# Optimization experiments

Measured on AMD Instinct MI355X. Metric: run time of the kernel, lower is better.

The kernel has to match this reference:

```python
import jax, jax.numpy as jnp
import numpy as np

B, S, HID = 2, 2048, 2048
NH, HD, G = 16, 128, 4
NKV = NH // G  # 4
ROPE_THETA = 10000.0


def _xavier(key, shape):
    fan_in, fan_out = shape
    lim = float(np.sqrt(6.0 / (fan_in + fan_out)))
    return jax.random.uniform(key, shape, jnp.float32, -lim, lim)


def setup_inputs() -> dict:
    key = jax.random.key(0)
    ks = jax.random.split(key, 6)
    hidden_states = jax.random.normal(ks[0], (B, S, HID), jnp.float32)
    # mask==True means MASKED (code adds mask * -1e9): causal upper triangle
    causal = jnp.triu(jnp.ones((S, S), jnp.bool_), k=1)
    mask = jnp.broadcast_to(causal[None, None], (B, 1, S, S))
    return {
        "hidden_states": hidden_states,
        "mask": mask,
        "Wq": _xavier(ks[1], (HID, NH * HD)),
        "bq": jnp.zeros((NH * HD,), jnp.float32),
        "Wk": _xavier(ks[2], (HID, NKV * HD)),
        "bk": jnp.zeros((NKV * HD,), jnp.float32),
        "Wv": _xavier(ks[3], (HID, NKV * HD)),
        "bv": jnp.zeros((NKV * HD,), jnp.float32),
        "Wo": _xavier(ks[4], (NH * HD, HID)),
        "bo": jnp.zeros((HID,), jnp.float32),
    }


def _rope_cos_sin(seq_len, head_dim, dtype):
    half = head_dim // 2
    inv_freq = 1.0 / (ROPE_THETA ** (jnp.arange(0, half, dtype=jnp.float32) / half))
    ang = jnp.arange(seq_len, dtype=jnp.float32)[:, None] * inv_freq[None, :]  # [S, half]
    # shape [1, S, 1, half] for broadcasting over (B, S, H, half)
    return jnp.cos(ang)[None, :, None, :].astype(dtype), jnp.sin(ang)[None, :, None, :].astype(dtype)


def _apply_rope(x, cos, sin):
    half = x.shape[-1] // 2
    x1, x2 = x[..., :half], x[..., half:]
    return jnp.concatenate([x1 * cos - x2 * sin, x1 * sin + x2 * cos], axis=-1)


def reference(hidden_states, mask, Wq, bq, Wk, bk, Wv, bv, Wo, bo):
    b, s, _ = hidden_states.shape
    scale = 1.0 / jnp.sqrt(jnp.asarray(HD, hidden_states.dtype))

    q = (hidden_states @ Wq + bq).reshape(b, s, NH, HD)
    k = (hidden_states @ Wk + bk).reshape(b, s, NKV, HD)
    v = (hidden_states @ Wv + bv).reshape(b, s, NKV, HD)

    cos, sin = _rope_cos_sin(s, HD, hidden_states.dtype)
    q = _apply_rope(q, cos, sin)
    k = _apply_rope(k, cos, sin)

    q = jnp.transpose(q, (0, 2, 1, 3))          # [B, NH, S, D]
    k = jnp.transpose(k, (0, 2, 1, 3))          # [B, NKV, S, D]
    v = jnp.transpose(v, (0, 2, 1, 3))          # [B, NKV, S, D]

    # GQA: group query heads instead of repeating K/V (same math as jnp.repeat)
    qg = q.reshape(b, NKV, G, s, HD)
    scores = jnp.einsum('bngqd,bnkd->bngqk', qg, k) * scale  # [B, NKV, G, S, S]

    maskf = mask.astype(scores.dtype)[:, :, None]  # [B, 1, 1, S, S]
    scores = scores + maskf * (-1e9)

    probs = jax.nn.softmax(scores, axis=-1)
    out = jnp.einsum('bngqk,bnkd->bngqd', probs, v)          # [B, NKV, G, S, D]
    out = out.reshape(b, NH, s, HD).transpose(0, 2, 1, 3).reshape(b, s, NH * HD)
    return out @ Wo + bo
```

## Files before the change

kernel.cpp:

```cpp
#include <hip/hip_runtime.h>
#include <hip/hip_bf16.h>

#define B_ 2
#define S_ 2048
#define HID_ 2048
#define NH_ 16
#define HD_ 128
#define NKV_ 4
#define M_ (B_*S_)
#define NQKV_ 3072
#define QSCALE2 0.12752464484148957f
#define DEFER_THR 11.5425f
#define NSPLIT 4

typedef __bf16 bf16x8 __attribute__((ext_vector_type(8)));
typedef float f32x4 __attribute__((ext_vector_type(4)));
typedef float f32x16 __attribute__((ext_vector_type(16)));

typedef __attribute__((address_space(1))) const unsigned int gas_uint;
typedef __attribute__((address_space(3))) unsigned int las_uint;

__device__ __forceinline__ unsigned short f2bfu(float x) {
  __hip_bfloat16 h = __float2bfloat16(x);
  return __builtin_bit_cast(unsigned short, h);
}

__device__ __forceinline__ unsigned int pack2bf(float lo, float hi) {
  return (unsigned int)f2bfu(lo) | ((unsigned int)f2bfu(hi) << 16);
}

__device__ __forceinline__ float bflo(unsigned int u) {
  return __builtin_bit_cast(float, u << 16);
}
__device__ __forceinline__ float bfhi(unsigned int u) {
  return __builtin_bit_cast(float, u & 0xffff0000u);
}
__device__ __forceinline__ float bf2f(unsigned short u) {
  return __builtin_bit_cast(float, (unsigned int)u << 16);
}

__device__ __forceinline__ void gload_lds16(const void* g, void* l) {
  __builtin_amdgcn_global_load_lds((gas_uint*)g, (las_uint*)l, 16, 0, 0);
}


__global__ void k_prep(const float* __restrict__ X, unsigned short* __restrict__ Xb,
                       const float* __restrict__ bq, const float* __restrict__ bk,
                       const float* __restrict__ bv, float* __restrict__ Bqkv,
                       float* __restrict__ cosT, float* __restrict__ sinT) {
  int blk = blockIdx.x;
  if (blk < 8192) {
    int i = blk * 256 + threadIdx.x;
    float4 v = ((const float4*)X)[i];
    ushort4 o;
    o.x = f2bfu(v.x); o.y = f2bfu(v.y); o.z = f2bfu(v.z); o.w = f2bfu(v.w);
    ((ushort4*)Xb)[i] = o;
  } else if (blk < 8204) {
    int i = (blk - 8192) * 256 + threadIdx.x;
    float v = (i < 2048) ? bq[i] : (i < 2560 ? bk[i - 2048] : bv[i - 2560]);
    Bqkv[i] = v;
  } else {
    int idx = (blk - 8204) * 256 + threadIdx.x;
    int s = idx >> 6, i = idx & 63;
    float invf = expf(-(float)i * (9.210340371976184f / 64.f));
    float ang = (float)s * invf;
    cosT[idx] = cosf(ang);
    sinT[idx] = sinf(ang);
  }
}

__global__ void k_tcvtall(const float* __restrict__ Wq, const float* __restrict__ Wk,
                          const float* __restrict__ Wv, const float* __restrict__ Wo,
                          unsigned short* __restrict__ Wt, unsigned short* __restrict__ Wot) {
  __shared__ float t[32][33];
  int blk = blockIdx.x;
  const float* src;
  unsigned short* dst;
  int R, C, bx, by;
  if (blk < 4096)      { src = Wq; dst = Wt;              R = 2048; C = 2048; int i = blk;        bx = i & 63; by = i >> 6; }
  else if (blk < 5120) { src = Wk; dst = Wt + 2048*2048;  R = 2048; C = 512;  int i = blk - 4096; bx = i & 15; by = i >> 4; }
  else if (blk < 6144) { src = Wv; dst = Wt + 2560*2048;  R = 2048; C = 512;  int i = blk - 5120; bx = i & 15; by = i >> 4; }
  else                 { src = Wo; dst = Wot;             R = 2048; C = 2048; int i = blk - 6144; bx = i & 63; by = i >> 6; }
  int bc = bx * 32, br = by * 32;
  int tx = threadIdx.x & 31, ty = threadIdx.x >> 5;
  for (int i = ty; i < 32; i += 8)
    t[i][tx] = src[(size_t)(br + i) * C + bc + tx];
  __syncthreads();
  for (int i = ty; i < 32; i += 8)
    dst[(size_t)(bc + i) * R + br + tx] = f2bfu(t[tx][i]);
}

__global__ void k_vt(const unsigned short* __restrict__ Cq, unsigned short* __restrict__ Vt) {
  __shared__ unsigned short t[32][136];
  int bx = blockIdx.x;
  int st = bx & 63, kv = (bx >> 6) & 3, b = bx >> 8;
  int s0 = st * 32;
  int tid = threadIdx.x;
  for (int j = 0; j < 16; ++j) {
    int idx = j * 256 + tid;
    int si = idx >> 7, d = idx & 127;
    t[si][d] = Cq[(size_t)(b * S_ + s0 + si) * NQKV_ + 2560 + kv * HD_ + d];
  }
  __syncthreads();
  for (int j = 0; j < 16; ++j) {
    int idx = j * 256 + tid;
    int d = idx >> 5, si = idx & 31;
    Vt[((size_t)(b * NKV_ + kv) * HD_ + d) * S_ + s0 + si] = t[si][d];
  }
}


template <int MODE>
__global__ __launch_bounds__(256, 2)
void k_gemm(const unsigned short* __restrict__ A, const unsigned short* __restrict__ Bt,
            const float* __restrict__ bias, void* __restrict__ Cv,
            int Md, int Nd, int Kd,
            const float* __restrict__ cosT, const float* __restrict__ sinT,
            unsigned short* __restrict__ Qr, unsigned short* __restrict__ Kr) {
  __shared__ __align__(16) unsigned short As[128 * 64];
  __shared__ __align__(16) unsigned short Bs[128 * 64];
  int nt = Nd >> 7;
  int nwg = (Md >> 7) * nt;
  int bid = blockIdx.x;
  int wg = bid;
  if ((nwg & 7) == 0) { int cpx = nwg >> 3; wg = (bid & 7) * cpx + (bid >> 3); }
  int bm = wg / nt, bn = wg - bm * nt;
  int tid = threadIdx.x;
  int lane = tid & 63, w = tid >> 6;
  int lr = lane & 15, lg = lane >> 4;
  f32x4 acc[2][8] = {};

  const int chunkbase = w << 2;
  const int boff = lane << 4;
  const int nK = Kd >> 6;
  const size_t rowstride = (size_t)Kd * 2;

  for (int kt = 0; kt < nK; ++kt) {
#pragma unroll
    for (int i = 0; i < 4; ++i) {
      int off = ((chunkbase + i) << 10) + boff;
      int row = off >> 7;
      int colb = off & 127;
      int scolb = colb ^ ((row & 7) << 4);
      const char* ga = (const char*)A + (size_t)(bm * 128 + row) * rowstride + (kt << 7) + scolb;
      const char* gb = (const char*)Bt + (size_t)(bn * 128 + row) * rowstride + (kt << 7) + scolb;
      gload_lds16(ga, (char*)As + ((chunkbase + i) << 10));
      gload_lds16(gb, (char*)Bs + ((chunkbase + i) << 10));
    }
    __syncthreads();
#pragma unroll
    for (int kk = 0; kk < 2; ++kk) {
      bf16x8 a[2], b[8];
      int kb = ((kk << 5) + (lg << 3)) << 1;
#pragma unroll
      for (int mi = 0; mi < 2; ++mi) {
        int row = (w << 5) + (mi << 4) + lr;
        a[mi] = *(const bf16x8*)((const char*)As + (row << 7) + (kb ^ ((row & 7) << 4)));
      }
#pragma unroll
      for (int ni = 0; ni < 8; ++ni) {
        int row = (ni << 4) + lr;
        b[ni] = *(const bf16x8*)((const char*)Bs + (row << 7) + (kb ^ ((row & 7) << 4)));
      }
#pragma unroll
      for (int mi = 0; mi < 2; ++mi)
#pragma unroll
        for (int ni = 0; ni < 8; ++ni)
          acc[mi][ni] = __builtin_amdgcn_mfma_f32_16x16x32_bf16(a[mi], b[ni], acc[mi][ni], 0, 0, 0);
    }
    __syncthreads();
  }

  if (MODE == 0 || bn >= 20) {
#pragma unroll
    for (int mi = 0; mi < 2; ++mi) {
      int r0 = bm * 128 + (w << 5) + (mi << 4) + (lg << 2);
#pragma unroll
      for (int ni = 0; ni < 8; ++ni) {
        int col = bn * 128 + (ni << 4) + lr;
        float bz = bias[col];
#pragma unroll
        for (int r = 0; r < 4; ++r) {
          float v = acc[mi][ni][r] + bz;
          if (MODE == 1)
            ((unsigned short*)Cv)[(size_t)(r0 + r) * Nd + col] = f2bfu(v);
          else
            ((float*)Cv)[(size_t)(r0 + r) * Nd + col] = v;
        }
      }
    }
  } else {
    bool isQ = (bn < 16);
    int hh = isQ ? bn : bn - 16;
#pragma unroll
    for (int mi = 0; mi < 2; ++mi) {
#pragma unroll
      for (int r = 0; r < 4; ++r) {
        int m = bm * 128 + (w << 5) + (mi << 4) + (lg << 2) + r;
        int s = m & (S_ - 1), bb = m >> 11;
        size_t qbase = ((size_t)(bb * NH_ + hh) * S_ + s) * HD_;
        size_t kbase = ((size_t)(bb * NKV_ + hh) * S_ + s) * HD_;
#pragma unroll
        for (int ni = 0; ni < 4; ++ni) {
          int c = (ni << 4) + lr;
          float v1 = acc[mi][ni][r]     + bias[bn * 128 + c];
          float v2 = acc[mi][ni + 4][r] + bias[bn * 128 + c + 64];
          float cs = cosT[(s << 6) + c], sn = sinT[(s << 6) + c];
          float o1 = v1 * cs - v2 * sn;
          float o2 = v1 * sn + v2 * cs;
          if (isQ) {
            Qr[qbase + c]      = f2bfu(o1 * QSCALE2);
            Qr[qbase + c + 64] = f2bfu(o2 * QSCALE2);
          } else {
            Kr[kbase + c]      = f2bfu(o1);
            Kr[kbase + c + 64] = f2bfu(o2);
          }
        }
      }
    }
  }
}


__global__ __launch_bounds__(256, 2)
void k_attn(const unsigned short* __restrict__ Qr, const unsigned short* __restrict__ Kr,
            const unsigned short* __restrict__ Vt,
            unsigned short* __restrict__ Po0, unsigned short* __restrict__ Po1,
            unsigned short* __restrict__ Po2, unsigned short* __restrict__ Po3,
            float2* __restrict__ Ml) {
  __shared__ __align__(16) unsigned short Ks[2][64 * 128];
  int bid = blockIdx.x;
  int g = bid & 7;
  int b = g >> 2, kvh = g & 3;
  int r = bid >> 3;
  int split = r & 3;
  int r2 = r >> 2;
  int hg = r2 >> 4;
  int qt = 15 - (r2 & 15);
  int h = (kvh << 2) + hg;
  int tid = threadIdx.x, lane = tid & 63, w = tid >> 6;
  int ql = lane & 31, hi = lane >> 5;
  int q0 = (qt << 7) + (w << 5);
  int qrow = q0 + ql;

  const unsigned short* Qp = Qr + (((size_t)(b * NH_ + h) * S_) << 7);
  const unsigned short* Kp = Kr + (((size_t)(b * NKV_ + kvh) * S_) << 7);
  const unsigned short* Vp = Vt + (((size_t)(b * NKV_ + kvh) * HD_) << 11);

  bf16x8 qa[8];
#pragma unroll
  for (int c = 0; c < 8; ++c)
    qa[c] = *(const bf16x8*)(Qp + (((size_t)qrow) << 7) + (c << 4) + (hi << 3));

  f32x16 acc[4] = {};
  float m_r = -1e30f, l_r = 0.f;

  const int T = (qt + 1) << 1;
  const int nit = (T - split + 3) >> 2;

#define STAGE_K(bsel, t)                                                        \
  {                                                                             \
    const char* kbase = (const char*)Kp + ((size_t)(t) << 14);                  \
    _Pragma("unroll")                                                           \
    for (int i_ = 0; i_ < 4; ++i_) {                                            \
      int woff_ = (i_ << 12) + (w << 10);                                       \
      int off_ = woff_ + (lane << 4);                                           \
      int row_ = off_ >> 8;                                                     \
      int colb_ = off_ & 255;                                                   \
      int scolb_ = colb_ ^ ((row_ & 15) << 4);                                  \
      gload_lds16(kbase + ((size_t)row_ << 8) + scolb_,                         \
                  (char*)Ks[bsel] + woff_);                                     \
    }                                                                           \
  }

  STAGE_K(0, split);
  __syncthreads();

  for (int i = 0; i < nit; ++i) {
    int t = split + (i << 2);
    if (i + 1 < nit) STAGE_K((i + 1) & 1, t + 4);
    const char* Kb = (const char*)Ks[i & 1];

#pragma unroll
    for (int sub = 0; sub < 2; ++sub) {
      int kvbase = (t << 6) + (sub << 5);
      if (kvbase > q0 + 31) continue;

      f32x16 st = {};
      int krow = (sub << 5) + ql;
      int sw = (krow & 15) << 4;
#pragma unroll
      for (int c = 0; c < 8; ++c) {
        int cb = (c << 5) + (hi << 4);
        bf16x8 kf = *(const bf16x8*)(Kb + (krow << 8) + (cb ^ sw));
        st = __builtin_amdgcn_mfma_f32_32x32x16_bf16(kf, qa[c], st, 0, 0, 0);
      }
      bf16x8 vf[8];
#pragma unroll
      for (int dc = 0; dc < 4; ++dc) {
        const unsigned short* vrow = Vp + (((size_t)((dc << 5) + ql)) << 11) + kvbase + (hi << 3);
        vf[2 * dc]     = *(const bf16x8*)(vrow);
        vf[2 * dc + 1] = *(const bf16x8*)(vrow + 16);
      }
      if (kvbase + 31 > q0) {
#pragma unroll
        for (int rr = 0; rr < 16; ++rr) {
          int kv = kvbase + (rr & 3) + ((rr >> 2) << 3) + (hi << 2);
          if (kv > qrow) st[rr] = -1e30f;
        }
      }
      float pmax = st[0];
#pragma unroll
      for (int rr = 1; rr < 16; ++rr) pmax = fmaxf(pmax, st[rr]);
      pmax = fmaxf(pmax, __shfl_xor(pmax, 32));
      if (!__all(pmax <= m_r + DEFER_THR)) {
        float mn = fmaxf(m_r, pmax);
        float al = exp2f(m_r - mn);
        m_r = mn;
        l_r *= al;
#pragma unroll
        for (int dc = 0; dc < 4; ++dc) acc[dc] = acc[dc] * al;
      }
      float p[16];
      float ps = 0.f;
#pragma unroll
      for (int rr = 0; rr < 16; ++rr) { p[rr] = exp2f(st[rr] - m_r); ps += p[rr]; }
      l_r += ps;
      unsigned int W[8];
#pragma unroll
      for (int i2 = 0; i2 < 8; ++i2) W[i2] = pack2bf(p[2 * i2], p[2 * i2 + 1]);
      unsigned int e0 = __shfl_xor(hi ? W[0] : W[2], 32);
      unsigned int e1 = __shfl_xor(hi ? W[1] : W[3], 32);
      unsigned int e2 = __shfl_xor(hi ? W[4] : W[6], 32);
      unsigned int e3 = __shfl_xor(hi ? W[5] : W[7], 32);
      uint4 u0, u1;
      u0.x = hi ? e0 : W[0];
      u0.y = hi ? e1 : W[1];
      u0.z = hi ? W[2] : e0;
      u0.w = hi ? W[3] : e1;
      u1.x = hi ? e2 : W[4];
      u1.y = hi ? e3 : W[5];
      u1.z = hi ? W[6] : e2;
      u1.w = hi ? W[7] : e3;
      bf16x8 pa0 = __builtin_bit_cast(bf16x8, u0);
      bf16x8 pa1 = __builtin_bit_cast(bf16x8, u1);
#pragma unroll
      for (int dc = 0; dc < 4; ++dc) {
        acc[dc] = __builtin_amdgcn_mfma_f32_32x32x16_bf16(vf[2 * dc], pa0, acc[dc], 0, 0, 0);
        acc[dc] = __builtin_amdgcn_mfma_f32_32x32x16_bf16(vf[2 * dc + 1], pa1, acc[dc], 0, 0, 0);
      }
    }
    __syncthreads();
  }

  float l_tot = l_r + __shfl_xor(l_r, 32);
  unsigned short* Pob = (split == 0) ? Po0 : (split == 1) ? Po1 : (split == 2) ? Po2 : Po3;
  float inv = (l_tot > 0.f) ? (1.f / l_tot) : 0.f;
  unsigned short* obase = Pob + ((((size_t)(b * S_) + qrow)) << 11) + (h << 7) + (hi << 2);
#pragma unroll
  for (int dc = 0; dc < 4; ++dc)
#pragma unroll
    for (int gq = 0; gq < 4; ++gq) {
      ushort4 o;
      o.x = f2bfu(acc[dc][4 * gq + 0] * inv);
      o.y = f2bfu(acc[dc][4 * gq + 1] * inv);
      o.z = f2bfu(acc[dc][4 * gq + 2] * inv);
      o.w = f2bfu(acc[dc][4 * gq + 3] * inv);
      *(ushort4*)(obase + (dc << 5) + (gq << 3)) = o;
    }
  if (hi == 0)
    Ml[(size_t)split * (M_ * NH_) + ((size_t)(b * S_) + qrow) * NH_ + h] = make_float2(m_r, l_tot);
}

__global__ void k_comb(const unsigned short* __restrict__ Po0, const unsigned short* __restrict__ Po1,
                       const unsigned short* __restrict__ Po2, const unsigned short* __restrict__ Po3,
                       const float2* __restrict__ Ml, unsigned short* __restrict__ Ob) {
  int idx = blockIdx.x * 256 + threadIdx.x;
  int c = idx >> 4;
  float2 a0 = Ml[c], a1 = Ml[c + M_ * NH_], a2 = Ml[c + 2 * M_ * NH_], a3 = Ml[c + 3 * M_ * NH_];
  float m = fmaxf(fmaxf(a0.x, a1.x), fmaxf(a2.x, a3.x));
  float w0 = a0.y * exp2f(a0.x - m);
  float w1 = a1.y * exp2f(a1.x - m);
  float w2 = a2.y * exp2f(a2.x - m);
  float w3 = a3.y * exp2f(a3.x - m);
  float inv = 1.f / (w0 + w1 + w2 + w3);
  w0 *= inv; w1 *= inv; w2 *= inv; w3 *= inv;
  size_t e = (size_t)idx << 3;
  uint4 v0 = *(const uint4*)(Po0 + e);
  uint4 v1 = *(const uint4*)(Po1 + e);
  uint4 v2 = *(const uint4*)(Po2 + e);
  uint4 v3 = *(const uint4*)(Po3 + e);
  uint4 o;
  o.x = pack2bf(w0 * bflo(v0.x) + w1 * bflo(v1.x) + w2 * bflo(v2.x) + w3 * bflo(v3.x),
                w0 * bfhi(v0.x) + w1 * bfhi(v1.x) + w2 * bfhi(v2.x) + w3 * bfhi(v3.x));
  o.y = pack2bf(w0 * bflo(v0.y) + w1 * bflo(v1.y) + w2 * bflo(v2.y) + w3 * bflo(v3.y),
                w0 * bfhi(v0.y) + w1 * bfhi(v1.y) + w2 * bfhi(v2.y) + w3 * bfhi(v3.y));
  o.z = pack2bf(w0 * bflo(v0.z) + w1 * bflo(v1.z) + w2 * bflo(v2.z) + w3 * bflo(v3.z),
                w0 * bfhi(v0.z) + w1 * bfhi(v1.z) + w2 * bfhi(v2.z) + w3 * bfhi(v3.z));
  o.w = pack2bf(w0 * bflo(v0.w) + w1 * bflo(v1.w) + w2 * bflo(v2.w) + w3 * bflo(v3.w),
                w0 * bfhi(v0.w) + w1 * bfhi(v1.w) + w2 * bfhi(v2.w) + w3 * bfhi(v3.w));
  *(uint4*)(Ob + e) = o;
}


extern "C" void kernel_launch(void* const* d_in, const int* in_sizes, int n_in,
                              void* d_out, int out_size, void* d_ws, size_t ws_size,
                              hipStream_t stream) {
  const float* X  = (const float*)d_in[0];
  const float* Wq = (const float*)d_in[2];
  const float* bq = (const float*)d_in[3];
  const float* Wk = (const float*)d_in[4];
  const float* bk = (const float*)d_in[5];
  const float* Wv = (const float*)d_in[6];
  const float* bv = (const float*)d_in[7];
  const float* Wo = (const float*)d_in[8];
  const float* bo = (const float*)d_in[9];
  float* out = (float*)d_out;

  char* ws = (char*)d_ws;
  unsigned short* Xb  = (unsigned short*)(ws);
  unsigned short* Wt  = (unsigned short*)(ws + 16777216);
  unsigned short* Wot = (unsigned short*)(ws + 29360128);
  float* Bqkv         = (float*)(ws + 37748736);
  float* cosT         = (float*)(ws + 37761024);
  float* sinT         = (float*)(ws + 38285312);
  unsigned short* Cqkvb = (unsigned short*)(ws + 38809600);
  unsigned short* Qr  = (unsigned short*)(ws + 89141248);
  unsigned short* Kr  = (unsigned short*)(ws + 105918464);
  unsigned short* Vtb = (unsigned short*)(ws + 110112768);
  unsigned short* Ob  = (unsigned short*)(ws + 114307072);
  unsigned short* Po0 = (unsigned short*)(ws);
  unsigned short* Po1 = (unsigned short*)(ws + 38809600);
  unsigned short* Po2 = (unsigned short*)(ws + 38809600 + 16777216);
  unsigned short* Po3 = (unsigned short*)(ws + 38809600 + 33554432);
  float2* Ml          = (float2*)(ws + 16777216);

  k_prep<<<8716, 256, 0, stream>>>(X, Xb, bq, bk, bv, Bqkv, cosT, sinT);
  k_tcvtall<<<10240, 256, 0, stream>>>(Wq, Wk, Wv, Wo, Wt, Wot);

  k_gemm<1><<<(M_ / 128) * (NQKV_ / 128), 256, 0, stream>>>(
      Xb, Wt, Bqkv, Cqkvb, M_, NQKV_, HID_, cosT, sinT, Qr, Kr);

  k_vt<<<B_ * NKV_ * (S_ / 32), 256, 0, stream>>>(Cqkvb, Vtb);

  k_attn<<<B_ * NH_ * (S_ / 128) * NSPLIT, 256, 0, stream>>>(Qr, Kr, Vtb, Po0, Po1, Po2, Po3, Ml);
  k_comb<<<M_ * HID_ / 8 / 256, 256, 0, stream>>>(Po0, Po1, Po2, Po3, Ml, Ob);

  k_gemm<0><<<(M_ / 128) * (HID_ / 128), 256, 0, stream>>>(
      Ob, Wot, bo, out, M_, HID_, NH_ * HD_, nullptr, nullptr, nullptr, nullptr);
}
```

Baseline: 232.7 us.

## Switch GEMM to 32x32x16 MFMA tiles and merge prep with weight transpose

The GEMM inner loop moves from 16x16x32 MFMA with 2x8 accumulator tiles to 32x32x16 MFMA with four 16-wide accumulators per wave. This cuts the number of LDS fragment loads and MFMA issues per K step. Both epilogues (plain bias store and the RoPE Q/K scatter) are remapped to the 32x32 output register layout. Separately, the weight transpose/convert kernel is folded into the prep kernel as extra blocks, which removes one launch and lets the two independent jobs overlap.

```diff
diff --git a/kernel.cpp b/kernel.cpp
--- a/kernel.cpp
+++ b/kernel.cpp
@@ -43,11 +43,14 @@
   __builtin_amdgcn_global_load_lds((gas_uint*)g, (las_uint*)l, 16, 0, 0);
 }
 
-
 __global__ void k_prep(const float* __restrict__ X, unsigned short* __restrict__ Xb,
                        const float* __restrict__ bq, const float* __restrict__ bk,
                        const float* __restrict__ bv, float* __restrict__ Bqkv,
-                       float* __restrict__ cosT, float* __restrict__ sinT) {
+                       float* __restrict__ cosT, float* __restrict__ sinT,
+                       const float* __restrict__ Wq, const float* __restrict__ Wk,
+                       const float* __restrict__ Wv, const float* __restrict__ Wo,
+                       unsigned short* __restrict__ Wt, unsigned short* __restrict__ Wot) {
+  __shared__ float t[32][33];
   int blk = blockIdx.x;
   if (blk < 8192) {
     int i = blk * 256 + threadIdx.x;
@@ -59,35 +62,30 @@
     int i = (blk - 8192) * 256 + threadIdx.x;
     float v = (i < 2048) ? bq[i] : (i < 2560 ? bk[i - 2048] : bv[i - 2560]);
     Bqkv[i] = v;
-  } else {
+  } else if (blk < 8716) {
     int idx = (blk - 8204) * 256 + threadIdx.x;
     int s = idx >> 6, i = idx & 63;
     float invf = expf(-(float)i * (9.210340371976184f / 64.f));
     float ang = (float)s * invf;
     cosT[idx] = cosf(ang);
     sinT[idx] = sinf(ang);
-  }
-}
-
-__global__ void k_tcvtall(const float* __restrict__ Wq, const float* __restrict__ Wk,
-                          const float* __restrict__ Wv, const float* __restrict__ Wo,
-                          unsigned short* __restrict__ Wt, unsigned short* __restrict__ Wot) {
-  __shared__ float t[32][33];
-  int blk = blockIdx.x;
-  const float* src;
-  unsigned short* dst;
-  int R, C, bx, by;
-  if (blk < 4096)      { src = Wq; dst = Wt;              R = 2048; C = 2048; int i = blk;        bx = i & 63; by = i >> 6; }
-  else if (blk < 5120) { src = Wk; dst = Wt + 2048*2048;  R = 2048; C = 512;  int i = blk - 4096; bx = i & 15; by = i >> 4; }
-  else if (blk < 6144) { src = Wv; dst = Wt + 2560*2048;  R = 2048; C = 512;  int i = blk - 5120; bx = i & 15; by = i >> 4; }
-  else                 { src = Wo; dst = Wot;             R = 2048; C = 2048; int i = blk - 6144; bx = i & 63; by = i >> 6; }
-  int bc = bx * 32, br = by * 32;
-  int tx = threadIdx.x & 31, ty = threadIdx.x >> 5;
-  for (int i = ty; i < 32; i += 8)
-    t[i][tx] = src[(size_t)(br + i) * C + bc + tx];
-  __syncthreads();
-  for (int i = ty; i < 32; i += 8)
-    dst[(size_t)(bc + i) * R + br + tx] = f2bfu(t[tx][i]);
+  } else {
+    int tb = blk - 8716;
+    const float* src;
+    unsigned short* dst;
+    int R, C, bx, by;
+    if (tb < 4096)      { src = Wq; dst = Wt;              R = 2048; C = 2048; bx = tb & 63;          by = tb >> 6; }
+    else if (tb < 5120) { src = Wk; dst = Wt + 2048*2048;  R = 2048; C = 512;  int i = tb - 4096; bx = i & 15; by = i >> 4; }
+    else if (tb < 6144) { src = Wv; dst = Wt + 2560*2048;  R = 2048; C = 512;  int i = tb - 5120; bx = i & 15; by = i >> 4; }
+    else                { src = Wo; dst = Wot;             R = 2048; C = 2048; int i = tb - 6144; bx = i & 63; by = i >> 6; }
+    int bc = bx * 32, br = by * 32;
+    int tx = threadIdx.x & 31, ty = threadIdx.x >> 5;
+    for (int i = ty; i < 32; i += 8)
+      t[i][tx] = src[(size_t)(br + i) * C + bc + tx];
+    __syncthreads();
+    for (int i = ty; i < 32; i += 8)
+      dst[(size_t)(bc + i) * R + br + tx] = f2bfu(t[tx][i]);
+  }
 }
 
 __global__ void k_vt(const unsigned short* __restrict__ Cq, unsigned short* __restrict__ Vt) {
@@ -127,13 +125,15 @@
   int bm = wg / nt, bn = wg - bm * nt;
   int tid = threadIdx.x;
   int lane = tid & 63, w = tid >> 6;
-  int lr = lane & 15, lg = lane >> 4;
-  f32x4 acc[2][8] = {};
+  int ql = lane & 31, hi = lane >> 5;
+  f32x16 acc[4] = {};
 
   const int chunkbase = w << 2;
   const int boff = lane << 4;
   const int nK = Kd >> 6;
   const size_t rowstride = (size_t)Kd * 2;
+  const int arow = (w << 5) + ql;
+  const int aswz = (arow & 7) << 4;
 
   for (int kt = 0; kt < nK; ++kt) {
 #pragma unroll
@@ -149,72 +149,57 @@
     }
     __syncthreads();
 #pragma unroll
-    for (int kk = 0; kk < 2; ++kk) {
-      bf16x8 a[2], b[8];
-      int kb = ((kk << 5) + (lg << 3)) << 1;
-#pragma unroll
-      for (int mi = 0; mi < 2; ++mi) {
-        int row = (w << 5) + (mi << 4) + lr;
-        a[mi] = *(const bf16x8*)((const char*)As + (row << 7) + (kb ^ ((row & 7) << 4)));
-      }
-#pragma unroll
-      for (int ni = 0; ni < 8; ++ni) {
-        int row = (ni << 4) + lr;
-        b[ni] = *(const bf16x8*)((const char*)Bs + (row << 7) + (kb ^ ((row & 7) << 4)));
-      }
-#pragma unroll
-      for (int mi = 0; mi < 2; ++mi)
-#pragma unroll
-        for (int ni = 0; ni < 8; ++ni)
-          acc[mi][ni] = __builtin_amdgcn_mfma_f32_16x16x32_bf16(a[mi], b[ni], acc[mi][ni], 0, 0, 0);
+    for (int ks = 0; ks < 4; ++ks) {
+      int kb = (ks << 5) + (hi << 4);
+      bf16x8 af = *(const bf16x8*)((const char*)As + (arow << 7) + (kb ^ aswz));
+#pragma unroll
+      for (int ni = 0; ni < 4; ++ni) {
+        int brow = (ni << 5) + ql;
+        bf16x8 bf = *(const bf16x8*)((const char*)Bs + (brow << 7) + (kb ^ ((brow & 7) << 4)));
+        acc[ni] = __builtin_amdgcn_mfma_f32_32x32x16_bf16(af, bf, acc[ni], 0, 0, 0);
+      }
     }
     __syncthreads();
   }
 
   if (MODE == 0 || bn >= 20) {
 #pragma unroll
-    for (int mi = 0; mi < 2; ++mi) {
-      int r0 = bm * 128 + (w << 5) + (mi << 4) + (lg << 2);
-#pragma unroll
-      for (int ni = 0; ni < 8; ++ni) {
-        int col = bn * 128 + (ni << 4) + lr;
-        float bz = bias[col];
-#pragma unroll
-        for (int r = 0; r < 4; ++r) {
-          float v = acc[mi][ni][r] + bz;
-          if (MODE == 1)
-            ((unsigned short*)Cv)[(size_t)(r0 + r) * Nd + col] = f2bfu(v);
-          else
-            ((float*)Cv)[(size_t)(r0 + r) * Nd + col] = v;
-        }
+    for (int ni = 0; ni < 4; ++ni) {
+      int col = bn * 128 + (ni << 5) + ql;
+      float bz = bias[col];
+#pragma unroll
+      for (int r = 0; r < 16; ++r) {
+        int m = bm * 128 + (w << 5) + (r & 3) + ((r >> 2) << 3) + (hi << 2);
+        float v = acc[ni][r] + bz;
+        if (MODE == 1)
+          ((unsigned short*)Cv)[(size_t)m * Nd + col] = f2bfu(v);
+        else
+          ((float*)Cv)[(size_t)m * Nd + col] = v;
       }
     }
   } else {
     bool isQ = (bn < 16);
     int hh = isQ ? bn : bn - 16;
 #pragma unroll
-    for (int mi = 0; mi < 2; ++mi) {
-#pragma unroll
-      for (int r = 0; r < 4; ++r) {
-        int m = bm * 128 + (w << 5) + (mi << 4) + (lg << 2) + r;
-        int s = m & (S_ - 1), bb = m >> 11;
-        size_t qbase = ((size_t)(bb * NH_ + hh) * S_ + s) * HD_;
-        size_t kbase = ((size_t)(bb * NKV_ + hh) * S_ + s) * HD_;
-#pragma unroll
-        for (int ni = 0; ni < 4; ++ni) {
-          int c = (ni << 4) + lr;
-          float v1 = acc[mi][ni][r]     + bias[bn * 128 + c];
-          float v2 = acc[mi][ni + 4][r] + bias[bn * 128 + c + 64];
-          float cs = cosT[(s << 6) + c], sn = sinT[(s << 6) + c];
-          float o1 = v1 * cs - v2 * sn;
-          float o2 = v1 * sn + v2 * cs;
-          if (isQ) {
-            Qr[qbase + c]      = f2bfu(o1 * QSCALE2);
-            Qr[qbase + c + 64] = f2bfu(o2 * QSCALE2);
-          } else {
-            Kr[kbase + c]      = f2bfu(o1);
-            Kr[kbase + c + 64] = f2bfu(o2);
-          }
+    for (int r = 0; r < 16; ++r) {
+      int m = bm * 128 + (w << 5) + (r & 3) + ((r >> 2) << 3) + (hi << 2);
+      int s = m & (S_ - 1), bb = m >> 11;
+      size_t base = isQ ? ((size_t)(bb * NH_ + hh) * S_ + s) * HD_
+                        : ((size_t)(bb * NKV_ + hh) * S_ + s) * HD_;
+#pragma unroll
+      for (int ni = 0; ni < 2; ++ni) {
+        int c = (ni << 5) + ql;
+        float v1 = acc[ni][r]     + bias[bn * 128 + c];
+        float v2 = acc[ni + 2][r] + bias[bn * 128 + c + 64];
+        float cs = cosT[(s << 6) + c], sn = sinT[(s << 6) + c];
+        float o1 = v1 * cs - v2 * sn;
+        float o2 = v1 * sn + v2 * cs;
+        if (isQ) {
+          Qr[base + c]      = f2bfu(o1 * QSCALE2);
+          Qr[base + c + 64] = f2bfu(o2 * QSCALE2);
+        } else {
+          Kr[base + c]      = f2bfu(o1);
+          Kr[base + c + 64] = f2bfu(o2);
         }
       }
     }
@@ -435,8 +420,8 @@
   unsigned short* Po3 = (unsigned short*)(ws + 38809600 + 33554432);
   float2* Ml          = (float2*)(ws + 16777216);
 
-  k_prep<<<8716, 256, 0, stream>>>(X, Xb, bq, bk, bv, Bqkv, cosT, sinT);
-  k_tcvtall<<<10240, 256, 0, stream>>>(Wq, Wk, Wv, Wo, Wt, Wot);
+  k_prep<<<18956, 256, 0, stream>>>(X, Xb, bq, bk, bv, Bqkv, cosT, sinT,
+                                    Wq, Wk, Wv, Wo, Wt, Wot);
 
   k_gemm<1><<<(M_ / 128) * (NQKV_ / 128), 256, 0, stream>>>(
       Xb, Wt, Bqkv, Cqkvb, M_, NQKV_, HID_, cosT, sinT, Qr, Kr);
```

Result: slower. 239.6 us (+3.0%).
